# Performance work log

Hardware: AMD Instinct MI355X
Metric: run time of the kernel (lower is better)

Reference implementation:

```python
import jax, jax.numpy as jnp
import numpy as np

B, S, E, H = 2, 4096, 512, 8
D = E // H  # head_dim = 64


def setup_inputs() -> dict:
    key = jax.random.key(0)
    ks = jax.random.split(key, 5)
    s = E ** -0.5
    return {
        "x": jax.random.normal(ks[0], (B, S, E), dtype=jnp.float32),
        "w_qkv": jax.random.normal(ks[1], (E, 3 * E), dtype=jnp.float32) * s,
        "b_qkv": jnp.zeros((3 * E,), dtype=jnp.float32),
        "w_out": jax.random.normal(ks[2], (E, E), dtype=jnp.float32) * s,
        "b_out": jnp.zeros((E,), dtype=jnp.float32),
    }


def reference(x, w_qkv, b_qkv, w_out, b_out):
    # qkv projection: [B,S,3E] -> [3,B,H,S,D]
    qkv = (x @ w_qkv + b_qkv).reshape(B, S, 3, H, D).transpose(2, 0, 3, 1, 4)
    q, k, v = qkv[0], qkv[1], qkv[2]
    # full score matrix [B,H,S,S] (faithful to the unfused torch impl)
    attn = jnp.einsum("bhqd,bhkd->bhqk", q, k) * (D ** -0.5)
    attn = jax.nn.softmax(attn, axis=-1)
    # dropout in eval mode -> identity (deterministic reference)
    out = jnp.einsum("bhqk,bhkd->bhqd", attn, v)  # [B,H,S,D]
    out = out.transpose(0, 2, 1, 3).reshape(B, S, E)
    return out @ w_out + b_out
```

## Files before the change

kernel.cpp:

```cpp
#include <hip/hip_runtime.h>
#include <hip/hip_bf16.h>

typedef __attribute__((ext_vector_type(8))) short bf16x8;
typedef __attribute__((ext_vector_type(4))) float f32x4;

#define MFMA16 __builtin_amdgcn_mfma_f32_16x16x32_bf16

__device__ __forceinline__ unsigned short f2bf(float f) {
  unsigned int u = __builtin_bit_cast(unsigned int, f);
  u += 0x7FFFu + ((u >> 16) & 1u);
  return (unsigned short)(u >> 16);
}

__device__ __forceinline__ void load_lds16(const void* g, void* l) {
  __builtin_amdgcn_global_load_lds(
      (const __attribute__((address_space(1))) unsigned int*)g,
      (__attribute__((address_space(3))) unsigned int*)l, 16, 0, 0);
}

__global__ __launch_bounds__(256) void prep_kernel(
    const float* __restrict__ x, const float* __restrict__ wqkv,
    const float* __restrict__ wout, unsigned short* __restrict__ xb,
    unsigned short* __restrict__ wqkvT, unsigned short* __restrict__ woutT) {
  int blk = blockIdx.x;
  int t = threadIdx.x;
  if (blk < 4096) {
    int i = (blk * 256 + t) * 4;
    float4 v = *(const float4*)(x + i);
    ushort4 o;
    o.x = f2bf(v.x); o.y = f2bf(v.y); o.z = f2bf(v.z); o.w = f2bf(v.w);
    *(ushort4*)(xb + i) = o;
  } else if (blk < 4864) {
    int u = ((blk - 4096) * 256 + t) * 4;
    int k = u / 1536, n = u % 1536;
    float4 v = *(const float4*)(wqkv + (size_t)k * 1536 + n);
    wqkvT[(size_t)(n + 0) * 512 + k] = f2bf(v.x);
    wqkvT[(size_t)(n + 1) * 512 + k] = f2bf(v.y);
    wqkvT[(size_t)(n + 2) * 512 + k] = f2bf(v.z);
    wqkvT[(size_t)(n + 3) * 512 + k] = f2bf(v.w);
  } else {
    int u = ((blk - 4864) * 256 + t) * 4;
    int k = u >> 9, n = u & 511;
    float4 v = *(const float4*)(wout + (size_t)k * 512 + n);
    woutT[(size_t)(n + 0) * 512 + k] = f2bf(v.x);
    woutT[(size_t)(n + 1) * 512 + k] = f2bf(v.y);
    woutT[(size_t)(n + 2) * 512 + k] = f2bf(v.z);
    woutT[(size_t)(n + 3) * 512 + k] = f2bf(v.w);
  }
}

__global__ __launch_bounds__(256, 2) void qkv_gemm(
    const unsigned short* __restrict__ xb, const unsigned short* __restrict__ bt,
    const float* __restrict__ bias, unsigned short* __restrict__ qout,
    unsigned short* __restrict__ ksw, unsigned short* __restrict__ vtsw) {
  __shared__ unsigned short SH[16384];
  const int t = threadIdx.x;
  const int lane = t & 63;
  const int llo = lane & 15, lhi = lane >> 4;
  const int w = t >> 6, wr = w >> 1, wc = w & 1;
  const int m0 = blockIdx.x * 128, n0 = blockIdx.y * 128;

  f32x4 acc[4][4];
#pragma unroll
  for (int i = 0; i < 4; ++i)
#pragma unroll
    for (int j = 0; j < 4; ++j) acc[i][j] = (f32x4){0.f, 0.f, 0.f, 0.f};

  const int r0 = t >> 2;
  const int sb = (t & 3) * 16;

  auto stage = [&](int k0, int buf) {
    const char* ga = (const char*)xb + (size_t)(m0 + r0) * 1024 + k0 * 2 + sb;
    const char* gb = (const char*)bt + (size_t)(n0 + r0) * 1024 + k0 * 2 + sb;
    char* la = (char*)SH + buf * 8192;
    char* lb = (char*)SH + 16384 + buf * 8192;
    load_lds16(ga, la + t * 16);
    load_lds16(ga + 64 * 1024, la + 4096 + t * 16);
    load_lds16(gb, lb + t * 16);
    load_lds16(gb + 64 * 1024, lb + 4096 + t * 16);
  };

  stage(0, 0);
  __syncthreads();

  int cur = 0;
  for (int k0 = 0; k0 < 512; k0 += 32) {
    if (k0 + 32 < 512) stage(k0 + 32, cur ^ 1);

    const unsigned short* usA = SH + cur * 4096;
    const unsigned short* usB = SH + 8192 + cur * 4096;
    bf16x8 af[4], bf[4];
#pragma unroll
    for (int mi = 0; mi < 4; ++mi)
      af[mi] = *(const bf16x8*)(usA + (wr * 64 + mi * 16 + llo) * 32 + lhi * 8);
#pragma unroll
    for (int ni = 0; ni < 4; ++ni)
      bf[ni] = *(const bf16x8*)(usB + (wc * 64 + ni * 16 + llo) * 32 + lhi * 8);
#pragma unroll
    for (int mi = 0; mi < 4; ++mi)
#pragma unroll
      for (int ni = 0; ni < 4; ++ni)
        acc[mi][ni] = MFMA16(af[mi], bf[ni], acc[mi][ni], 0, 0, 0);
    __syncthreads();
    cur ^= 1;
  }

  const int sec = n0 >> 9;
  const int hbase = (n0 >> 6) & 7;
#pragma unroll
  for (int ni = 0; ni < 4; ++ni) {
    int lcol = wc * 64 + ni * 16 + llo;
    float bv = bias[n0 + lcol];
#pragma unroll
    for (int mi = 0; mi < 4; ++mi) {
#pragma unroll
      for (int r = 0; r < 4; ++r) {
        int rowm = wr * 64 + mi * 16 + lhi * 4 + r;
        float val = acc[mi][ni][r] + bv;
        unsigned short bits;
        int idx;
        if (sec == 0) {
          bits = f2bf(val * 0.18033688f);
          idx = rowm * 128 + (lcol ^ ((rowm & 15) << 3));
        } else if (sec == 1) {
          bits = f2bf(val);
          idx = rowm * 128 + (lcol ^ ((rowm & 15) << 3));
        } else {
          bits = f2bf(val);
          int u64k = rowm & 63;
          int c = u64k >> 4, u = u64k & 15;
          int kperm = ((c >> 1) << 5) + ((u >> 2) << 3) + ((c & 1) << 2) + (u & 3);
          int ktile = rowm >> 6;
          idx = lcol * 128 + ((ktile * 64 + kperm) ^ ((lcol & 15) << 3));
        }
        SH[idx] = bits;
      }
    }
  }
  __syncthreads();

  const int b = m0 >> 12;
  if (sec == 0) {
#pragma unroll
    for (int j = 0; j < 8; ++j) {
      int cidx = j * 256 + t;
      int dc = cidx & 7, srow = (cidx >> 3) & 127, h2 = cidx >> 10;
      int bh = b * 8 + hbase + h2;
      int s = (m0 & 4095) + srow;
      bf16x8 v = *(const bf16x8*)(SH + srow * 128 +
                                  ((h2 * 64 + dc * 8) ^ ((srow & 15) << 3)));
      *(bf16x8*)(qout + ((size_t)bh * 4096 + s) * 64 + dc * 8) = v;
    }
  } else if (sec == 1) {
#pragma unroll
    for (int j = 0; j < 8; ++j) {
      int cidx = j * 256 + t;
      int dc = cidx & 7, srow = (cidx >> 3) & 127, h2 = cidx >> 10;
      int bh = b * 8 + hbase + h2;
      int s = (m0 & 4095) + srow;
      bf16x8 v = *(const bf16x8*)(SH + srow * 128 +
                                  ((h2 * 64 + dc * 8) ^ ((srow & 15) << 3)));
      size_t byte = (size_t)bh * 524288 + (size_t)(s >> 6) * 8192 +
                    (size_t)(s & 63) * 128 + ((dc * 16) ^ ((s & 7) << 4));
      *(bf16x8*)((char*)ksw + byte) = v;
    }
  } else {
#pragma unroll
    for (int j = 0; j < 8; ++j) {
      int cidx = j * 256 + t;
      int dc = cidx & 7, drow = (cidx >> 3) & 63;
      int ktile = (cidx >> 9) & 1, h2 = cidx >> 10;
      int bh = b * 8 + hbase + h2;
      int lcol = h2 * 64 + drow;
      bf16x8 v = *(const bf16x8*)(SH + lcol * 128 +
                                  ((ktile * 64 + dc * 8) ^ ((lcol & 15) << 3)));
      size_t byte = (size_t)bh * 524288 +
                    (size_t)(((m0 & 4095) >> 6) + ktile) * 8192 +
                    (size_t)drow * 128 + ((dc * 16) ^ ((drow & 7) << 4));
      *(bf16x8*)((char*)vtsw + byte) = v;
    }
  }
}

__global__ __launch_bounds__(256, 2) void attn_kernel(
    const unsigned short* __restrict__ qp, const unsigned short* __restrict__ ksw,
    const unsigned short* __restrict__ vtsw, unsigned short* __restrict__ aout) {
  __shared__ unsigned short Ks[2][4096];
  __shared__ unsigned short Vts[2][4096];

  const int t = threadIdx.x, lane = t & 63, w = t >> 6;
  const int llo = lane & 15, lhi = lane >> 4;

  const int wg = blockIdx.x + (blockIdx.y << 5);
  const int pidx = ((wg & 7) << 6) + (wg >> 3);
  const int bh = pidx >> 5;
  const int q0 = (pidx & 31) * 128 + w * 32;

  bf16x8 qf[2][2];
#pragma unroll
  for (int qs = 0; qs < 2; ++qs)
#pragma unroll
    for (int f = 0; f < 2; ++f) {
      int row = q0 + qs * 16 + llo;
      int d = f * 32 + lhi * 8;
      qf[qs][f] = *(const bf16x8*)(qp + ((size_t)bh * 4096 + row) * 64 + d);
    }

  float lpart[2] = {0.f, 0.f};
  f32x4 o[2][4];
#pragma unroll
  for (int qs = 0; qs < 2; ++qs)
#pragma unroll
    for (int di = 0; di < 4; ++di) o[qs][di] = (f32x4){0.f, 0.f, 0.f, 0.f};

  const char* kbase = (const char*)ksw + (size_t)bh * 524288;
  const char* vbase = (const char*)vtsw + (size_t)bh * 524288;

  bf16x8 pf[2][2];

  auto stage_tile = [&](const char* g, char* d) {
    load_lds16(g + t * 16, d + t * 16);
    load_lds16(g + 4096 + t * 16, d + 4096 + t * 16);
  };

  auto qkt = [&](f32x4 (&sc)[2][4], const char* kbuf) {
    __builtin_amdgcn_s_setprio(1);
#pragma unroll
    for (int c = 0; c < 4; ++c) {
      int krow = c * 16 + llo;
      int sw = (krow & 7) << 4;
      bf16x8 kf0 = *(const bf16x8*)(kbuf + krow * 128 + ((lhi * 16) ^ sw));
      bf16x8 kf1 = *(const bf16x8*)(kbuf + krow * 128 + ((lhi * 16 + 64) ^ sw));
#pragma unroll
      for (int qs = 0; qs < 2; ++qs) {
        sc[qs][c] = MFMA16(kf0, qf[qs][0], (f32x4){0.f, 0.f, 0.f, 0.f}, 0, 0, 0);
        sc[qs][c] = MFMA16(kf1, qf[qs][1], sc[qs][c], 0, 0, 0);
      }
    }
    __builtin_amdgcn_s_setprio(0);
  };

  auto softmax_pack = [&](f32x4 (&sc)[2][4]) {
#pragma unroll
    for (int qs = 0; qs < 2; ++qs) {
      float e[4][4];
#pragma unroll
      for (int c = 0; c < 4; ++c)
#pragma unroll
        for (int r = 0; r < 4; ++r) {
          e[c][r] = __builtin_amdgcn_exp2f(sc[qs][c][r]);
          lpart[qs] += e[c][r];
        }
#pragma unroll
      for (int f = 0; f < 2; ++f) {
        bf16x8 pvv;
#pragma unroll
        for (int j = 0; j < 8; ++j)
          pvv[j] = __builtin_bit_cast(short,
                       __float2bfloat16(e[2 * f + (j >> 2)][j & 3]));
        pf[qs][f] = pvv;
      }
    }
  };

  auto pv_accum = [&](const char* vbuf) {
    __builtin_amdgcn_s_setprio(1);
#pragma unroll
    for (int f = 0; f < 2; ++f)
#pragma unroll
      for (int di = 0; di < 4; ++di) {
        int vrow = di * 16 + llo;
        int byte = vrow * 128 + ((lhi * 16 + f * 64) ^ ((vrow & 7) << 4));
        bf16x8 vf = *(const bf16x8*)(vbuf + byte);
#pragma unroll
        for (int qs = 0; qs < 2; ++qs)
          o[qs][di] = MFMA16(pf[qs][f], vf, o[qs][di], 0, 0, 0);
      }
    __builtin_amdgcn_s_setprio(0);
  };

  stage_tile(kbase, (char*)&Ks[0][0]);
  stage_tile(vbase, (char*)&Vts[0][0]);
  stage_tile(kbase + 8192, (char*)&Ks[1][0]);
  __syncthreads();

  f32x4 scA[2][4], scB[2][4];
  qkt(scA, (const char*)&Ks[0][0]);
  __syncthreads();

  for (int kt = 0; kt < 62; kt += 2) {
    stage_tile(kbase + (size_t)(kt + 2) * 8192, (char*)&Ks[0][0]);
    stage_tile(vbase + (size_t)(kt + 1) * 8192, (char*)&Vts[1][0]);
    qkt(scB, (const char*)&Ks[1][0]);
    softmax_pack(scA);
    pv_accum((const char*)&Vts[0][0]);
    __syncthreads();
    stage_tile(kbase + (size_t)(kt + 3) * 8192, (char*)&Ks[1][0]);
    stage_tile(vbase + (size_t)(kt + 2) * 8192, (char*)&Vts[0][0]);
    qkt(scA, (const char*)&Ks[0][0]);
    softmax_pack(scB);
    pv_accum((const char*)&Vts[1][0]);
    __syncthreads();
  }

  stage_tile(vbase + (size_t)63 * 8192, (char*)&Vts[1][0]);
  qkt(scB, (const char*)&Ks[1][0]);
  softmax_pack(scA);
  pv_accum((const char*)&Vts[0][0]);
  __syncthreads();
  softmax_pack(scB);
  pv_accum((const char*)&Vts[1][0]);

  float linv[2][4];
#pragma unroll
  for (int qs = 0; qs < 2; ++qs) {
    float s = lpart[qs];
    s += __shfl_xor(s, 16, 64);
    s += __shfl_xor(s, 32, 64);
#pragma unroll
    for (int r = 0; r < 4; ++r)
      linv[qs][r] = 1.f / __shfl(s, lhi * 4 + r, 64);
  }

  int b = bh >> 3, h = bh & 7;
#pragma unroll
  for (int qs = 0; qs < 2; ++qs)
#pragma unroll
    for (int di = 0; di < 4; ++di)
#pragma unroll
      for (int r = 0; r < 4; ++r) {
        int s = q0 + qs * 16 + lhi * 4 + r;
        int d = di * 16 + llo;
        float val = o[qs][di][r] * linv[qs][r];
        aout[((size_t)b * 4096 + s) * 512 + h * 64 + d] = f2bf(val);
      }
}

__global__ __launch_bounds__(256, 2) void out_gemm(
    const unsigned short* __restrict__ ab, const unsigned short* __restrict__ bt,
    const float* __restrict__ bias, float* __restrict__ out) {
  __shared__ unsigned short As[2][128 * 32];
  __shared__ unsigned short Bs[2][64 * 32];
  const int t = threadIdx.x;
  const int lane = t & 63;
  const int llo = lane & 15, lhi = lane >> 4;
  const int w = t >> 6;
  const int m0 = blockIdx.x * 128, n0 = blockIdx.y * 64;

  f32x4 acc[2][4];
#pragma unroll
  for (int i = 0; i < 2; ++i)
#pragma unroll
    for (int j = 0; j < 4; ++j) acc[i][j] = (f32x4){0.f, 0.f, 0.f, 0.f};

  const int r0 = t >> 2;
  const int sb = (t & 3) * 16;

  auto stage = [&](int k0, int buf) {
    const char* ga = (const char*)ab + (size_t)(m0 + r0) * 1024 + k0 * 2 + sb;
    const char* gb = (const char*)bt + (size_t)(n0 + r0) * 1024 + k0 * 2 + sb;
    load_lds16(ga, (char*)&As[buf][0] + t * 16);
    load_lds16(ga + 64 * 1024, (char*)&As[buf][0] + 4096 + t * 16);
    load_lds16(gb, (char*)&Bs[buf][0] + t * 16);
  };

  stage(0, 0);
  __syncthreads();

  int cur = 0;
  for (int k0 = 0; k0 < 512; k0 += 32) {
    if (k0 + 32 < 512) stage(k0 + 32, cur ^ 1);

    bf16x8 af[2], bf[4];
#pragma unroll
    for (int mi = 0; mi < 2; ++mi)
      af[mi] = *(const bf16x8*)(&As[cur][0] + (w * 32 + mi * 16 + llo) * 32 + lhi * 8);
#pragma unroll
    for (int ni = 0; ni < 4; ++ni)
      bf[ni] = *(const bf16x8*)(&Bs[cur][0] + (ni * 16 + llo) * 32 + lhi * 8);
#pragma unroll
    for (int mi = 0; mi < 2; ++mi)
#pragma unroll
      for (int ni = 0; ni < 4; ++ni)
        acc[mi][ni] = MFMA16(af[mi], bf[ni], acc[mi][ni], 0, 0, 0);
    __syncthreads();
    cur ^= 1;
  }

#pragma unroll
  for (int ni = 0; ni < 4; ++ni) {
    int col = n0 + ni * 16 + llo;
    float bv = bias[col];
#pragma unroll
    for (int mi = 0; mi < 2; ++mi) {
      int rowb = m0 + w * 32 + mi * 16 + lhi * 4;
#pragma unroll
      for (int r = 0; r < 4; ++r)
        out[(size_t)(rowb + r) * 512 + col] = acc[mi][ni][r] + bv;
    }
  }
}

extern "C" void kernel_launch(void* const* d_in, const int* in_sizes, int n_in,
                              void* d_out, int out_size, void* d_ws, size_t ws_size,
                              hipStream_t stream) {
  const float* x = (const float*)d_in[0];
  const float* wqkv = (const float*)d_in[1];
  const float* bqkv = (const float*)d_in[2];
  const float* wout = (const float*)d_in[3];
  const float* bout = (const float*)d_in[4];
  float* out = (float*)d_out;

  char* ws = (char*)d_ws;
  unsigned short* xb    = (unsigned short*)(ws + 0);
  unsigned short* wqkvT = (unsigned short*)(ws + 8388608);
  unsigned short* woutT = (unsigned short*)(ws + 9961472);
  unsigned short* qb    = (unsigned short*)(ws + 10485760);
  unsigned short* ksw   = (unsigned short*)(ws + 18874368);
  unsigned short* vtsw  = (unsigned short*)(ws + 27262976);
  unsigned short* ab    = (unsigned short*)(ws + 35651584);
  (void)ws_size; (void)in_sizes; (void)n_in; (void)out_size;

  prep_kernel<<<5120, 256, 0, stream>>>(x, wqkv, wout, xb, wqkvT, woutT);
  qkv_gemm<<<dim3(64, 12), 256, 0, stream>>>(xb, wqkvT, bqkv, qb, ksw, vtsw);
  attn_kernel<<<dim3(32, 16), 256, 0, stream>>>(qb, ksw, vtsw, ab);
  out_gemm<<<dim3(64, 8), 256, 0, stream>>>(ab, woutT, bout, out);
}
```

Before: 129.4 us.

## Split attention KV range in two with a separate combine kernel

Each (batch, head, query-tile) is now processed by two workgroups, each covering half of the key/value sequence. The grid doubles and launch bounds allow four blocks per CU, to improve occupancy and latency hiding. Each split writes unnormalized bf16 partial outputs and row sums, and a new combine kernel adds them and normalizes into the activation buffer for the output GEMM. This costs an extra kernel launch, extra global traffic for the partials, and some bf16 rounding of unnormalized partials; workspace buffers are reused to hold the partials.

```diff
diff --git a/kernel.cpp b/kernel.cpp
--- a/kernel.cpp
+++ b/kernel.cpp
@@ -10,6 +10,11 @@
   unsigned int u = __builtin_bit_cast(unsigned int, f);
   u += 0x7FFFu + ((u >> 16) & 1u);
   return (unsigned short)(u >> 16);
+}
+
+__device__ __forceinline__ float bf2f(unsigned short b) {
+  unsigned int u = ((unsigned int)b) << 16;
+  return __builtin_bit_cast(float, u);
 }
 
 __device__ __forceinline__ void load_lds16(const void* g, void* l) {
@@ -182,19 +187,23 @@
   }
 }
 
-__global__ __launch_bounds__(256, 2) void attn_kernel(
+__global__ __launch_bounds__(256, 4) void attn_kernel(
     const unsigned short* __restrict__ qp, const unsigned short* __restrict__ ksw,
-    const unsigned short* __restrict__ vtsw, unsigned short* __restrict__ aout) {
+    const unsigned short* __restrict__ vtsw, unsigned short* __restrict__ po0,
+    unsigned short* __restrict__ po1, float* __restrict__ pl0,
+    float* __restrict__ pl1) {
   __shared__ unsigned short Ks[2][4096];
   __shared__ unsigned short Vts[2][4096];
 
   const int t = threadIdx.x, lane = t & 63, w = t >> 6;
   const int llo = lane & 15, lhi = lane >> 4;
 
-  const int wg = blockIdx.x + (blockIdx.y << 5);
-  const int pidx = ((wg & 7) << 6) + (wg >> 3);
-  const int bh = pidx >> 5;
-  const int q0 = (pidx & 31) * 128 + w * 32;
+  const int wg = blockIdx.x + (blockIdx.y << 6);
+  const int pidx = ((wg & 7) << 7) + (wg >> 3);
+  const int bh = pidx >> 6;
+  const int qt = (pidx & 63) >> 1;
+  const int split = pidx & 1;
+  const int q0 = qt * 128 + w * 32;
 
   bf16x8 qf[2][2];
 #pragma unroll
@@ -213,8 +222,8 @@
 #pragma unroll
     for (int di = 0; di < 4; ++di) o[qs][di] = (f32x4){0.f, 0.f, 0.f, 0.f};
 
-  const char* kbase = (const char*)ksw + (size_t)bh * 524288;
-  const char* vbase = (const char*)vtsw + (size_t)bh * 524288;
+  const char* kbase = (const char*)ksw + (size_t)bh * 524288 + (size_t)split * 262144;
+  const char* vbase = (const char*)vtsw + (size_t)bh * 524288 + (size_t)split * 262144;
 
   bf16x8 pf[2][2];
 
@@ -288,7 +297,7 @@
   qkt(scA, (const char*)&Ks[0][0]);
   __syncthreads();
 
-  for (int kt = 0; kt < 62; kt += 2) {
+  for (int kt = 0; kt < 30; kt += 2) {
     stage_tile(kbase + (size_t)(kt + 2) * 8192, (char*)&Ks[0][0]);
     stage_tile(vbase + (size_t)(kt + 1) * 8192, (char*)&Vts[1][0]);
     qkt(scB, (const char*)&Ks[1][0]);
@@ -303,7 +312,7 @@
     __syncthreads();
   }
 
-  stage_tile(vbase + (size_t)63 * 8192, (char*)&Vts[1][0]);
+  stage_tile(vbase + (size_t)31 * 8192, (char*)&Vts[1][0]);
   qkt(scB, (const char*)&Ks[1][0]);
   softmax_pack(scA);
   pv_accum((const char*)&Vts[0][0]);
@@ -311,29 +320,59 @@
   softmax_pack(scB);
   pv_accum((const char*)&Vts[1][0]);
 
-  float linv[2][4];
+  float lred[2];
 #pragma unroll
   for (int qs = 0; qs < 2; ++qs) {
     float s = lpart[qs];
     s += __shfl_xor(s, 16, 64);
     s += __shfl_xor(s, 32, 64);
-#pragma unroll
-    for (int r = 0; r < 4; ++r)
-      linv[qs][r] = 1.f / __shfl(s, lhi * 4 + r, 64);
-  }
-
-  int b = bh >> 3, h = bh & 7;
+    lred[qs] = s;
+  }
+
+  unsigned short* poX = split ? po1 : po0;
+  float* plX = split ? pl1 : pl0;
+  const size_t pb = ((size_t)bh * 32 + qt) * 8192;
 #pragma unroll
   for (int qs = 0; qs < 2; ++qs)
 #pragma unroll
     for (int di = 0; di < 4; ++di)
 #pragma unroll
       for (int r = 0; r < 4; ++r) {
-        int s = q0 + qs * 16 + lhi * 4 + r;
+        int row = w * 32 + qs * 16 + lhi * 4 + r;
         int d = di * 16 + llo;
-        float val = o[qs][di][r] * linv[qs][r];
-        aout[((size_t)b * 4096 + s) * 512 + h * 64 + d] = f2bf(val);
+        poX[pb + row * 64 + d] = f2bf(o[qs][di][r]);
       }
+  if (lhi == 0) {
+#pragma unroll
+    for (int qs = 0; qs < 2; ++qs)
+      plX[((size_t)bh * 32 + qt) * 128 + w * 32 + qs * 16 + llo] = lred[qs];
+  }
+}
+
+__global__ __launch_bounds__(256) void combine_kernel(
+    const unsigned short* __restrict__ po0, const unsigned short* __restrict__ po1,
+    const float* __restrict__ pl0, const float* __restrict__ pl1,
+    unsigned short* __restrict__ ab) {
+  int idx = blockIdx.x * 256 + threadIdx.x;
+  int m = idx >> 6;
+  int h = (idx >> 3) & 7;
+  int d0 = (idx & 7) * 8;
+  int b = m >> 12, s = m & 4095;
+  int qt = s >> 7, row = s & 127;
+  int bh = b * 8 + h;
+  size_t po = ((size_t)bh * 32 + qt) * 8192 + row * 64 + d0;
+  size_t pli = ((size_t)bh * 32 + qt) * 128 + row;
+
+  bf16x8 a = *(const bf16x8*)(po0 + po);
+  bf16x8 c = *(const bf16x8*)(po1 + po);
+  float linv = 1.f / (pl0[pli] + pl1[pli]);
+  bf16x8 r;
+#pragma unroll
+  for (int j = 0; j < 8; ++j) {
+    float v = (bf2f((unsigned short)a[j]) + bf2f((unsigned short)c[j])) * linv;
+    r[j] = __builtin_bit_cast(short, __float2bfloat16(v));
+  }
+  *(bf16x8*)(ab + (size_t)m * 512 + h * 64 + d0) = r;
 }
 
 __global__ __launch_bounds__(256, 2) void out_gemm(
@@ -418,11 +457,16 @@
   unsigned short* qb    = (unsigned short*)(ws + 10485760);
   unsigned short* ksw   = (unsigned short*)(ws + 18874368);
   unsigned short* vtsw  = (unsigned short*)(ws + 27262976);
-  unsigned short* ab    = (unsigned short*)(ws + 35651584);
+  unsigned short* po1   = (unsigned short*)(ws + 35651584);
+  float*          pl0   = (float*)(ws + 44040192);
+  float*          pl1   = (float*)(ws + 44302336);
+  unsigned short* po0   = xb;
+  unsigned short* ab    = qb;
   (void)ws_size; (void)in_sizes; (void)n_in; (void)out_size;
 
   prep_kernel<<<5120, 256, 0, stream>>>(x, wqkv, wout, xb, wqkvT, woutT);
   qkv_gemm<<<dim3(64, 12), 256, 0, stream>>>(xb, wqkvT, bqkv, qb, ksw, vtsw);
-  attn_kernel<<<dim3(32, 16), 256, 0, stream>>>(qb, ksw, vtsw, ab);
+  attn_kernel<<<dim3(64, 16), 256, 0, stream>>>(qb, ksw, vtsw, po0, po1, pl0, pl1);
+  combine_kernel<<<2048, 256, 0, stream>>>(po0, po1, pl0, pl1, ab);
   out_gemm<<<dim3(64, 8), 256, 0, stream>>>(ab, woutT, bout, out);
 }
```

New measurement: 343.2 us. 165% more time.

## Halve attention query tile per block to double grid and occupancy

Applied to the files above, without the earlier changes.

Each attention block now covers 64 queries instead of 128, with each wave computing 16 query rows instead of 32. The grid doubles to 1024 blocks and launch bounds rise to 4 blocks per SM, aiming for more resident waves and better coverage across the CUs. In exchange, each K/V tile staged in LDS is reused by half as many queries, so global K/V traffic and LDS loads per MFMA double.

```diff
diff --git a/kernel.cpp b/kernel.cpp
--- a/kernel.cpp
+++ b/kernel.cpp
@@ -182,7 +182,7 @@
   }
 }
 
-__global__ __launch_bounds__(256, 2) void attn_kernel(
+__global__ __launch_bounds__(256, 4) void attn_kernel(
     const unsigned short* __restrict__ qp, const unsigned short* __restrict__ ksw,
     const unsigned short* __restrict__ vtsw, unsigned short* __restrict__ aout) {
   __shared__ unsigned short Ks[2][4096];
@@ -191,39 +191,35 @@
   const int t = threadIdx.x, lane = t & 63, w = t >> 6;
   const int llo = lane & 15, lhi = lane >> 4;
 
-  const int wg = blockIdx.x + (blockIdx.y << 5);
-  const int pidx = ((wg & 7) << 6) + (wg >> 3);
-  const int bh = pidx >> 5;
-  const int q0 = (pidx & 31) * 128 + w * 32;
-
-  bf16x8 qf[2][2];
-#pragma unroll
-  for (int qs = 0; qs < 2; ++qs)
-#pragma unroll
-    for (int f = 0; f < 2; ++f) {
-      int row = q0 + qs * 16 + llo;
-      int d = f * 32 + lhi * 8;
-      qf[qs][f] = *(const bf16x8*)(qp + ((size_t)bh * 4096 + row) * 64 + d);
-    }
-
-  float lpart[2] = {0.f, 0.f};
-  f32x4 o[2][4];
-#pragma unroll
-  for (int qs = 0; qs < 2; ++qs)
-#pragma unroll
-    for (int di = 0; di < 4; ++di) o[qs][di] = (f32x4){0.f, 0.f, 0.f, 0.f};
+  const int wg = blockIdx.x + (blockIdx.y << 6);
+  const int pidx = ((wg & 7) << 7) + (wg >> 3);
+  const int bh = pidx >> 6;
+  const int q0 = (pidx & 63) * 64 + w * 16;
+
+  bf16x8 qf[2];
+#pragma unroll
+  for (int f = 0; f < 2; ++f) {
+    int row = q0 + llo;
+    int d = f * 32 + lhi * 8;
+    qf[f] = *(const bf16x8*)(qp + ((size_t)bh * 4096 + row) * 64 + d);
+  }
+
+  float lpart = 0.f;
+  f32x4 o[4];
+#pragma unroll
+  for (int di = 0; di < 4; ++di) o[di] = (f32x4){0.f, 0.f, 0.f, 0.f};
 
   const char* kbase = (const char*)ksw + (size_t)bh * 524288;
   const char* vbase = (const char*)vtsw + (size_t)bh * 524288;
 
-  bf16x8 pf[2][2];
+  bf16x8 pf[2];
 
   auto stage_tile = [&](const char* g, char* d) {
     load_lds16(g + t * 16, d + t * 16);
     load_lds16(g + 4096 + t * 16, d + 4096 + t * 16);
   };
 
-  auto qkt = [&](f32x4 (&sc)[2][4], const char* kbuf) {
+  auto qkt = [&](f32x4 (&sc)[4], const char* kbuf) {
     __builtin_amdgcn_s_setprio(1);
 #pragma unroll
     for (int c = 0; c < 4; ++c) {
@@ -231,35 +227,29 @@
       int sw = (krow & 7) << 4;
       bf16x8 kf0 = *(const bf16x8*)(kbuf + krow * 128 + ((lhi * 16) ^ sw));
       bf16x8 kf1 = *(const bf16x8*)(kbuf + krow * 128 + ((lhi * 16 + 64) ^ sw));
-#pragma unroll
-      for (int qs = 0; qs < 2; ++qs) {
-        sc[qs][c] = MFMA16(kf0, qf[qs][0], (f32x4){0.f, 0.f, 0.f, 0.f}, 0, 0, 0);
-        sc[qs][c] = MFMA16(kf1, qf[qs][1], sc[qs][c], 0, 0, 0);
+      sc[c] = MFMA16(kf0, qf[0], (f32x4){0.f, 0.f, 0.f, 0.f}, 0, 0, 0);
+      sc[c] = MFMA16(kf1, qf[1], sc[c], 0, 0, 0);
+    }
+    __builtin_amdgcn_s_setprio(0);
+  };
+
+  auto softmax_pack = [&](f32x4 (&sc)[4]) {
+    float e[4][4];
+#pragma unroll
+    for (int c = 0; c < 4; ++c)
+#pragma unroll
+      for (int r = 0; r < 4; ++r) {
+        e[c][r] = __builtin_amdgcn_exp2f(sc[c][r]);
+        lpart += e[c][r];
       }
-    }
-    __builtin_amdgcn_s_setprio(0);
-  };
-
-  auto softmax_pack = [&](f32x4 (&sc)[2][4]) {
-#pragma unroll
-    for (int qs = 0; qs < 2; ++qs) {
-      float e[4][4];
-#pragma unroll
-      for (int c = 0; c < 4; ++c)
-#pragma unroll
-        for (int r = 0; r < 4; ++r) {
-          e[c][r] = __builtin_amdgcn_exp2f(sc[qs][c][r]);
-          lpart[qs] += e[c][r];
-        }
-#pragma unroll
-      for (int f = 0; f < 2; ++f) {
-        bf16x8 pvv;
-#pragma unroll
-        for (int j = 0; j < 8; ++j)
-          pvv[j] = __builtin_bit_cast(short,
-                       __float2bfloat16(e[2 * f + (j >> 2)][j & 3]));
-        pf[qs][f] = pvv;
-      }
+#pragma unroll
+    for (int f = 0; f < 2; ++f) {
+      bf16x8 pvv;
+#pragma unroll
+      for (int j = 0; j < 8; ++j)
+        pvv[j] = __builtin_bit_cast(short,
+                     __float2bfloat16(e[2 * f + (j >> 2)][j & 3]));
+      pf[f] = pvv;
     }
   };
 
@@ -272,9 +262,7 @@
         int vrow = di * 16 + llo;
         int byte = vrow * 128 + ((lhi * 16 + f * 64) ^ ((vrow & 7) << 4));
         bf16x8 vf = *(const bf16x8*)(vbuf + byte);
-#pragma unroll
-        for (int qs = 0; qs < 2; ++qs)
-          o[qs][di] = MFMA16(pf[qs][f], vf, o[qs][di], 0, 0, 0);
+        o[di] = MFMA16(pf[f], vf, o[di], 0, 0, 0);
       }
     __builtin_amdgcn_s_setprio(0);
   };
@@ -284,7 +272,7 @@
   stage_tile(kbase + 8192, (char*)&Ks[1][0]);
   __syncthreads();
 
-  f32x4 scA[2][4], scB[2][4];
+  f32x4 scA[4], scB[4];
   qkt(scA, (const char*)&Ks[0][0]);
   __syncthreads();
 
@@ -311,29 +299,26 @@
   softmax_pack(scB);
   pv_accum((const char*)&Vts[1][0]);
 
-  float linv[2][4];
-#pragma unroll
-  for (int qs = 0; qs < 2; ++qs) {
-    float s = lpart[qs];
+  float linv[4];
+  {
+    float s = lpart;
     s += __shfl_xor(s, 16, 64);
     s += __shfl_xor(s, 32, 64);
 #pragma unroll
     for (int r = 0; r < 4; ++r)
-      linv[qs][r] = 1.f / __shfl(s, lhi * 4 + r, 64);
+      linv[r] = 1.f / __shfl(s, lhi * 4 + r, 64);
   }
 
   int b = bh >> 3, h = bh & 7;
 #pragma unroll
-  for (int qs = 0; qs < 2; ++qs)
-#pragma unroll
-    for (int di = 0; di < 4; ++di)
-#pragma unroll
-      for (int r = 0; r < 4; ++r) {
-        int s = q0 + qs * 16 + lhi * 4 + r;
-        int d = di * 16 + llo;
-        float val = o[qs][di][r] * linv[qs][r];
-        aout[((size_t)b * 4096 + s) * 512 + h * 64 + d] = f2bf(val);
-      }
+  for (int di = 0; di < 4; ++di)
+#pragma unroll
+    for (int r = 0; r < 4; ++r) {
+      int s = q0 + lhi * 4 + r;
+      int d = di * 16 + llo;
+      float val = o[di][r] * linv[r];
+      aout[((size_t)b * 4096 + s) * 512 + h * 64 + d] = f2bf(val);
+    }
 }
 
 __global__ __launch_bounds__(256, 2) void out_gemm(
@@ -423,6 +408,6 @@
 
   prep_kernel<<<5120, 256, 0, stream>>>(x, wqkv, wout, xb, wqkvT, woutT);
   qkv_gemm<<<dim3(64, 12), 256, 0, stream>>>(xb, wqkvT, bqkv, qb, ksw, vtsw);
-  attn_kernel<<<dim3(32, 16), 256, 0, stream>>>(qb, ksw, vtsw, ab);
+  attn_kernel<<<dim3(64, 16), 256, 0, stream>>>(qb, ksw, vtsw, ab);
   out_gemm<<<dim3(64, 8), 256, 0, stream>>>(ab, woutT, bout, out);
 }
```

New measurement: 135.9 us. +5.0%, slower.
